# Optimization experiments

Measured on AMD Instinct MI355X. Metric: run time of the kernel, lower is better.

The kernel has to match this reference:

```python
import jax, jax.numpy as jnp
import numpy as np

NEG = jnp.float32(-1e9)


def setup_inputs() -> dict:
    key = jax.random.key(0)
    ks = jax.random.split(key, 8)
    B, S, D = 8, 2048, 1024
    scale = 1.0 / np.sqrt(D)
    return {
        "xQ": jax.random.normal(ks[0], (B, S, D), jnp.float32),
        "xK": jax.random.normal(ks[1], (B, S, D), jnp.float32),
        "xV": jax.random.normal(ks[2], (B, S, D), jnp.float32),
        "padding_mask": jax.random.randint(ks[3], (B, S), 0, 2, jnp.int32),
        "casual_mask": jnp.ones((B, S), jnp.int32),
        "W_q": jax.random.normal(ks[4], (D, D), jnp.float32) * scale,
        "b_q": jnp.zeros((D,), jnp.float32),
        "W_k": jax.random.normal(ks[5], (D, D), jnp.float32) * scale,
        "b_k": jnp.zeros((D,), jnp.float32),
        "W_v": jax.random.normal(ks[6], (D, D), jnp.float32) * scale,
        "b_v": jnp.zeros((D,), jnp.float32),
    }


def reference(xQ, xK, xV, padding_mask, casual_mask, W_q, b_q, W_k, b_k, W_v, b_v):
    # Linear projections (torch nn.Linear: x @ W.T + b)
    Q = jnp.einsum('bsd,ed->bse', xQ, W_q) + b_q
    K = jnp.einsum('bsd,ed->bse', xK, W_k) + b_k
    V = jnp.einsum('bsd,ed->bse', xV, W_v) + b_v

    # Raw logits (note: original code applies NO 1/sqrt(dk) scaling)
    QKT = jnp.einsum('bqd,bkd->bqk', Q, K)  # [B, Sq, Sk]

    # Additive padding mask: -1e9 on padded key positions
    pad = jnp.where(padding_mask[:, None, :] == 0, NEG, jnp.float32(0.0))
    # Additive causal mask: -1e9 above the diagonal
    Sq, Sk = QKT.shape[1], QKT.shape[2]
    caus = jnp.where(
        jnp.tril(jnp.ones((Sq, Sk), dtype=bool)), jnp.float32(0.0), NEG
    )[None, :, :]
    QKT = QKT + pad + caus

    S = jax.nn.softmax(QKT, axis=-1)
    return jnp.einsum('bqk,bkd->bqd', S, V)
```

## Files before the change

kernel.cpp:

```cpp
#include <hip/hip_runtime.h>

typedef __attribute__((ext_vector_type(4))) float f4;
typedef __attribute__((ext_vector_type(4))) float f32x4;
typedef _Float16 half4 __attribute__((ext_vector_type(4)));
typedef _Float16 half8 __attribute__((ext_vector_type(8)));

#define DEVI static __device__ __forceinline__

DEVI void gload_lds16(const void* g, void* l) {
  __builtin_amdgcn_global_load_lds(
      (const __attribute__((address_space(1))) void*)g,
      (__attribute__((address_space(3))) void*)l, 16, 0, 0);
}

#define STEP_SYNC()                                     \
  asm volatile("s_waitcnt vmcnt(0)" ::: "memory");      \
  __builtin_amdgcn_sched_barrier(0);                    \
  __builtin_amdgcn_s_barrier();                         \
  __builtin_amdgcn_sched_barrier(0);

DEVI int xcd_swz(int id, int n) {
  int q = n >> 3, r = n & 7;
  int x = id & 7, c = id >> 3;
  return (x < r ? x * (q + 1) : r * (q + 1) + (x - r) * q) + c;
}

template <int SL>
__global__ __launch_bounds__(256) void cvt_split(const float* __restrict__ X,
                                                 _Float16* __restrict__ H,
                                                 _Float16* __restrict__ L,
                                                 int n4) {
  int i = blockIdx.x * 256 + threadIdx.x;
  const int stride = gridDim.x * 256;
  for (; i < n4; i += stride) {
    f4 x = ((const f4*)X)[i];
    half4 h, l;
#pragma unroll
    for (int j = 0; j < 4; ++j) {
      h[j] = (_Float16)x[j];
      if (SL) l[j] = (_Float16)(x[j] - (float)h[j]);
    }
    ((half4*)H)[i] = h;
    if (SL) ((half4*)L)[i] = l;
  }
}

template <int AR, int BR, int ASPLIT, int BSPLIT>
DEVI void core(const _Float16* __restrict__ A0, const _Float16* __restrict__ A1,
               const _Float16* __restrict__ B0, const _Float16* __restrict__ B1,
               int lda, int ldb, int NS, _Float16* lds, f32x4 (&acc)[4][4]) {
  constexpr int WN = BR / 64;
  constexpr int ACH = AR * 32;
  constexpr int BCH = BR * 32;
  constexpr int CHUNK = ACH * (1 + ASPLIT) + BCH * (1 + BSPLIT);
  const int tid = threadIdx.x;
  const int w = tid >> 6, lane = tid & 63;
  const int wm = w / WN, wn = w % WN;
  const int r16 = lane & 15, kg = lane >> 4;

  auto STAGE = [&](int t) {
    _Float16* base = lds + (size_t)(t & 1) * CHUNK;
#pragma unroll
    for (int j = 0; j < AR / 128; ++j) {
      int g = j * 512 + tid;
      int row = g >> 2, c = g & 3;
      int cs = (c ^ (row >> 1)) & 3;
      size_t src = (size_t)row * lda + cs * 8 + t * 32;
      int dst = (j * 512 + w * 64) * 8;
      gload_lds16(A0 + src, base + dst);
      if (ASPLIT) gload_lds16(A1 + src, base + ACH + dst);
    }
    _Float16* bb = base + ACH * (1 + ASPLIT);
#pragma unroll
    for (int j = 0; j < BR / 128; ++j) {
      int g = j * 512 + tid;
      int row = g >> 2, c = g & 3;
      int cs = (c ^ (row >> 1)) & 3;
      size_t src = (size_t)row * ldb + cs * 8 + t * 32;
      int dst = (j * 512 + w * 64) * 8;
      gload_lds16(B0 + src, bb + dst);
      if (BSPLIT) gload_lds16(B1 + src, bb + BCH + dst);
    }
  };

  auto COMPUTE = [&](int t) {
    const _Float16* base = lds + (size_t)(t & 1) * CHUNK;
    const _Float16* la = base;
    const _Float16* lb = base + ACH * (1 + ASPLIT);
    half8 a0[4], a1[4], b0[4], b1[4];
#pragma unroll
    for (int mi = 0; mi < 4; ++mi) {
      int row = wm * 64 + mi * 16 + r16;
      int off = row * 32 + (((kg ^ (row >> 1)) & 3) * 8);
      a0[mi] = *(const half8*)(la + off);
      if (ASPLIT) a1[mi] = *(const half8*)(la + ACH + off);
    }
#pragma unroll
    for (int ni = 0; ni < 4; ++ni) {
      int row = wn * 64 + ni * 16 + r16;
      int off = row * 32 + (((kg ^ (row >> 1)) & 3) * 8);
      b0[ni] = *(const half8*)(lb + off);
      if (BSPLIT) b1[ni] = *(const half8*)(lb + BCH + off);
    }
    __builtin_amdgcn_s_setprio(1);
#pragma unroll
    for (int mi = 0; mi < 4; ++mi)
#pragma unroll
      for (int ni = 0; ni < 4; ++ni) {
        acc[mi][ni] = __builtin_amdgcn_mfma_f32_16x16x32_f16(
            a0[mi], b0[ni], acc[mi][ni], 0, 0, 0);
        if (ASPLIT)
          acc[mi][ni] = __builtin_amdgcn_mfma_f32_16x16x32_f16(
              a1[mi], b0[ni], acc[mi][ni], 0, 0, 0);
        if (BSPLIT)
          acc[mi][ni] = __builtin_amdgcn_mfma_f32_16x16x32_f16(
              a0[mi], b1[ni], acc[mi][ni], 0, 0, 0);
      }
    __builtin_amdgcn_s_setprio(0);
  };

  STAGE(0);
  STEP_SYNC();
  for (int t = 0; t < NS; ++t) {
    if (t + 1 < NS) STAGE(t + 1);
    COMPUTE(t);
    STEP_SYNC();
  }
}

DEVI void acc_zero(f32x4 (&acc)[4][4]) {
#pragma unroll
  for (int i = 0; i < 4; ++i)
#pragma unroll
    for (int j = 0; j < 4; ++j) acc[i][j] = (f32x4)0.0f;
}

template <int STORE_LO>
__global__ __launch_bounds__(512, 4) void proj_eng(
    const _Float16* __restrict__ X, const _Float16* __restrict__ Wh,
    const _Float16* __restrict__ Wl, const float* __restrict__ bias,
    _Float16* __restrict__ OutHi, _Float16* __restrict__ OutLo) {
  extern __shared__ _Float16 lds[];
  const int id = xcd_swz(blockIdx.x, gridDim.x);
  const int m0 = (id >> 3) * 256, n0 = (id & 7) * 128;
  f32x4 acc[4][4];
  acc_zero(acc);
  core<256, 128, 0, 1>(X + (size_t)m0 * 1024, nullptr,
                       Wh + (size_t)n0 * 1024, Wl + (size_t)n0 * 1024, 1024,
                       1024, 32, lds, acc);
  const int tid = threadIdx.x;
  const int w = tid >> 6, lane = tid & 63;
  const int wm = w >> 1, wn = w & 1;
  const int r16 = lane & 15, kg = lane >> 4;
  float bcol[4];
#pragma unroll
  for (int ni = 0; ni < 4; ++ni) bcol[ni] = bias[n0 + wn * 64 + ni * 16 + r16];
#pragma unroll
  for (int mi = 0; mi < 4; ++mi) {
    int row = m0 + wm * 64 + mi * 16 + kg * 4;
#pragma unroll
    for (int ni = 0; ni < 4; ++ni) {
      int col = n0 + wn * 64 + ni * 16 + r16;
#pragma unroll
      for (int j = 0; j < 4; ++j) {
        float v = acc[mi][ni][j] + bcol[ni];
        _Float16 h = (_Float16)v;
        OutHi[(size_t)(row + j) * 1024 + col] = h;
        if (STORE_LO)
          OutLo[(size_t)(row + j) * 1024 + col] = (_Float16)(v - (float)h);
      }
    }
  }
}

__global__ __launch_bounds__(512, 4) void proj_eng_v(
    const _Float16* __restrict__ X, const _Float16* __restrict__ Wh,
    const float* __restrict__ bias, _Float16* __restrict__ Vt) {
  extern __shared__ _Float16 lds[];
  const int id = xcd_swz(blockIdx.x, gridDim.x);
  const int m0 = (id >> 3) * 256, n0 = (id & 7) * 128;
  f32x4 acc[4][4];
  acc_zero(acc);
  core<256, 128, 0, 0>(X + (size_t)m0 * 1024, nullptr,
                       Wh + (size_t)n0 * 1024, nullptr, 1024, 1024, 32, lds,
                       acc);
  const int tid = threadIdx.x;
  const int w = tid >> 6, lane = tid & 63;
  const int wm = w >> 1, wn = w & 1;
  const int r16 = lane & 15, kg = lane >> 4;
  float bcol[4];
#pragma unroll
  for (int ni = 0; ni < 4; ++ni) bcol[ni] = bias[n0 + wn * 64 + ni * 16 + r16];
  __syncthreads();
  _Float16(*T)[256] = (_Float16(*)[256])lds;
#pragma unroll
  for (int mi = 0; mi < 4; ++mi) {
    int ml = wm * 64 + mi * 16 + kg * 4;
#pragma unroll
    for (int ni = 0; ni < 4; ++ni) {
      int nl = wn * 64 + ni * 16 + r16;
#pragma unroll
      for (int j = 0; j < 4; ++j)
        T[nl][ml + j] = (_Float16)(acc[mi][ni][j] + bcol[ni]);
    }
  }
  __syncthreads();
  const int b = m0 >> 11;
  const int s0 = m0 & 2047;
#pragma unroll
  for (int r = 0; r < 8; ++r) {
    int flat = tid + r * 512;
    int n = flat >> 5, c = flat & 31;
    half8 v = *(const half8*)&T[n][c * 8];
    *(half8*)(Vt + (size_t)b * (1024 * 2048) + (size_t)(n0 + n) * 2048 + s0 +
              c * 8) = v;
  }
}

__global__ __launch_bounds__(512, 4) void qk_eng(
    const _Float16* __restrict__ Qh, const _Float16* __restrict__ Ql,
    const _Float16* __restrict__ Kh, float* __restrict__ Lg, int bbase) {
  extern __shared__ _Float16 lds[];
  const int id = xcd_swz(blockIdx.x, gridDim.x);
  const int y = id / 72;
  int t = id % 72;
  int qt = 0, base = 0;
  while (t >= base + (qt >> 1) + 1) { base += (qt >> 1) + 1; ++qt; }
  const int kt = t - base;
  const int b = bbase + y;
  const size_t boff = (size_t)b * (2048 * 1024);
  f32x4 acc[4][4];
  acc_zero(acc);
  core<128, 256, 1, 0>(Qh + boff + (size_t)(qt * 128) * 1024,
                       Ql + boff + (size_t)(qt * 128) * 1024,
                       Kh + boff + (size_t)(kt * 256) * 1024, nullptr, 1024,
                       1024, 32, lds, acc);
  const int tid = threadIdx.x;
  const int w = tid >> 6, lane = tid & 63;
  const int wm = w >> 2, wn = w & 3;
  const int r16 = lane & 15, kg = lane >> 4;
  float* L = Lg + (size_t)y * (2048 * 2048);
#pragma unroll
  for (int mi = 0; mi < 4; ++mi) {
    int row = qt * 128 + wm * 64 + mi * 16 + kg * 4;
#pragma unroll
    for (int ni = 0; ni < 4; ++ni) {
      int col = kt * 256 + wn * 64 + ni * 16 + r16;
#pragma unroll
      for (int j = 0; j < 4; ++j)
        L[(size_t)(row + j) * 2048 + col] = acc[mi][ni][j];
    }
  }
}

__global__ __launch_bounds__(512, 4) void pv_eng(
    const float* __restrict__ Lg, const _Float16* __restrict__ Vt,
    float* __restrict__ Out, int bbase) {
  extern __shared__ _Float16 lds[];
  const int id = xcd_swz(blockIdx.x, gridDim.x);
  const int y = id >> 6;
  const int qt = (id & 63) >> 2, nt = id & 3;
  const int b = bbase + y;
  const _Float16* P = (const _Float16*)(Lg + (size_t)y * (2048 * 2048));
  f32x4 acc[4][4];
  acc_zero(acc);
  core<128, 256, 0, 0>(P + (size_t)(qt * 128) * 4096, nullptr,
                       Vt + (size_t)b * (1024 * 2048) + (size_t)(nt * 256) * 2048,
                       nullptr, 4096, 2048, ((qt >> 1) + 1) * 8, lds, acc);
  const int tid = threadIdx.x;
  const int w = tid >> 6, lane = tid & 63;
  const int wm = w >> 2, wn = w & 3;
  const int r16 = lane & 15, kg = lane >> 4;
#pragma unroll
  for (int mi = 0; mi < 4; ++mi) {
    int row = qt * 128 + wm * 64 + mi * 16 + kg * 4;
#pragma unroll
    for (int ni = 0; ni < 4; ++ni) {
      int col = nt * 256 + wn * 64 + ni * 16 + r16;
#pragma unroll
      for (int j = 0; j < 4; ++j)
        Out[(size_t)(b * 2048 + row + j) * 1024 + col] = acc[mi][ni][j];
    }
  }
}

template <int NSPLIT, int STORE_LO>
__global__ __launch_bounds__(256) void proj_kernel(
    const float* __restrict__ X, const float* __restrict__ W,
    const float* __restrict__ bias, _Float16* __restrict__ OutHi,
    _Float16* __restrict__ OutLo) {
  __shared__ struct {
    float As[128][36];
    float Bs[128][36];
  } u;
  const int tid = threadIdx.x;
  const int lane = tid & 63, w = tid >> 6;
  const int wm = w >> 1, wn = w & 1;
  const int r16 = lane & 15, kg = lane >> 4;
  const int m0 = blockIdx.y * 128, n0 = blockIdx.x * 128;
  f32x4 acc[4][4];
#pragma unroll
  for (int i = 0; i < 4; ++i)
#pragma unroll
    for (int j = 0; j < 4; ++j) acc[i][j] = (f32x4)0.0f;
  f4 ra[4], rb[4];
  auto LOAD = [&](int kt) {
#pragma unroll
    for (int r = 0; r < 4; ++r) {
      int flat = tid + r * 256;
      int row = flat >> 3, c = flat & 7;
      ra[r] = *(const f4*)(X + (size_t)(m0 + row) * 1024 + kt * 32 + c * 4);
      rb[r] = *(const f4*)(W + (size_t)(n0 + row) * 1024 + kt * 32 + c * 4);
    }
  };
  LOAD(0);
  for (int kt = 0; kt < 32; ++kt) {
    __syncthreads();
#pragma unroll
    for (int r = 0; r < 4; ++r) {
      int flat = tid + r * 256;
      int row = flat >> 3, c = flat & 7;
      *(f4*)&u.As[row][c * 4] = ra[r];
      *(f4*)&u.Bs[row][c * 4] = rb[r];
    }
    __syncthreads();
    if (kt + 1 < 32) LOAD(kt + 1);
    half8 ah[4], al[4], bh[4];
#pragma unroll
    for (int mi = 0; mi < 4; ++mi) {
      const float* p = &u.As[wm * 64 + mi * 16 + r16][kg * 8];
      f4 x0 = *(const f4*)p, x1 = *(const f4*)(p + 4);
      half8 h, l;
#pragma unroll
      for (int j = 0; j < 4; ++j) {
        h[j] = (_Float16)x0[j];
        h[j + 4] = (_Float16)x1[j];
      }
      ah[mi] = h;
      if (NSPLIT == 2) {
#pragma unroll
        for (int j = 0; j < 4; ++j) {
          l[j] = (_Float16)(x0[j] - (float)h[j]);
          l[j + 4] = (_Float16)(x1[j] - (float)h[j + 4]);
        }
        al[mi] = l;
      }
    }
#pragma unroll
    for (int ni = 0; ni < 4; ++ni) {
      const float* p = &u.Bs[wn * 64 + ni * 16 + r16][kg * 8];
      f4 x0 = *(const f4*)p, x1 = *(const f4*)(p + 4);
      half8 h;
#pragma unroll
      for (int j = 0; j < 4; ++j) {
        h[j] = (_Float16)x0[j];
        h[j + 4] = (_Float16)x1[j];
      }
      bh[ni] = h;
    }
#pragma unroll
    for (int mi = 0; mi < 4; ++mi)
#pragma unroll
      for (int ni = 0; ni < 4; ++ni) {
        acc[mi][ni] = __builtin_amdgcn_mfma_f32_16x16x32_f16(
            ah[mi], bh[ni], acc[mi][ni], 0, 0, 0);
        if (NSPLIT == 2)
          acc[mi][ni] = __builtin_amdgcn_mfma_f32_16x16x32_f16(
              al[mi], bh[ni], acc[mi][ni], 0, 0, 0);
      }
  }
  float bcol[4];
#pragma unroll
  for (int ni = 0; ni < 4; ++ni) bcol[ni] = bias[n0 + wn * 64 + ni * 16 + r16];
#pragma unroll
  for (int mi = 0; mi < 4; ++mi) {
    int row = m0 + wm * 64 + mi * 16 + kg * 4;
#pragma unroll
    for (int ni = 0; ni < 4; ++ni) {
      int col = n0 + wn * 64 + ni * 16 + r16;
#pragma unroll
      for (int j = 0; j < 4; ++j) {
        float v = acc[mi][ni][j] + bcol[ni];
        _Float16 h = (_Float16)v;
        OutHi[(size_t)(row + j) * 1024 + col] = h;
        if (STORE_LO)
          OutLo[(size_t)(row + j) * 1024 + col] = (_Float16)(v - (float)h);
      }
    }
  }
}

__global__ __launch_bounds__(256) void softmax_kernel(
    float* __restrict__ Lg, const int* __restrict__ pad, int bbase) {
  const int q = blockIdx.x;
  const int y = blockIdx.y;
  const int b = bbase + y;
  const int tid = threadIdx.x;
  float* row = Lg + (size_t)y * (2048 * 2048) + (size_t)q * 2048;
  _Float16* prow = (_Float16*)row;
  const int* pb = pad + (size_t)b * 2048;
  const int kend = ((q >> 8) + 1) << 8;
  float v[8];
  int nv = 0;
  float mx = -3.0e38f;
  for (int k = tid; k <= q; k += 256) {
    float l = row[k];
    if (pb[k] == 0) l += -1.0e9f;
    v[nv++] = l;
    mx = fmaxf(mx, l);
  }
  __shared__ float red[4];
  for (int o = 32; o; o >>= 1) mx = fmaxf(mx, __shfl_xor(mx, o));
  if ((tid & 63) == 0) red[tid >> 6] = mx;
  __syncthreads();
  mx = fmaxf(fmaxf(red[0], red[1]), fmaxf(red[2], red[3]));
  __syncthreads();
  float s = 0.f;
  for (int i = 0; i < nv; ++i) s += expf(v[i] - mx);
  for (int o = 32; o; o >>= 1) s += __shfl_xor(s, o);
  if ((tid & 63) == 0) red[tid >> 6] = s;
  __syncthreads();
  s = red[0] + red[1] + red[2] + red[3];
  const float inv = 1.0f / s;
  int i = 0;
  for (int k = tid; k <= q; k += 256) {
    prow[k] = (_Float16)(expf(v[i] - mx) * inv);
    ++i;
  }
  for (int k = q + 1 + tid; k < kend; k += 256) prow[k] = (_Float16)0.0f;
}

__global__ __launch_bounds__(512) void fix_f(const int* __restrict__ pad,
                                             int* __restrict__ fb) {
  const int b = threadIdx.x >> 6, k = threadIdx.x & 63;
  unsigned long long m = __ballot(pad[b * 2048 + k] != 0);
  if (k == 0) fb[b] = m ? (__ffsll((long long)m) - 1) : 64;
}

__global__ __launch_bounds__(256) void fix_qrow2(
    const float* __restrict__ xQ, const float* __restrict__ Wq,
    const float* __restrict__ bq, const int* __restrict__ fb,
    float* __restrict__ Qrow) {
  const int b = blockIdx.y;
  const int f = fb[b];
  const int tid = threadIdx.x;
  const int e = blockIdx.x * 16 + (tid >> 4);
  const int l16 = tid & 15;
  __shared__ float xq[1024];
  for (int q = 0; q < f; ++q) {
    *(f4*)&xq[tid * 4] = ((const f4*)(xQ + (size_t)(b * 2048 + q) * 1024))[tid];
    __syncthreads();
    float a = 0.f;
#pragma unroll
    for (int it = 0; it < 16; ++it) {
      int d = l16 * 4 + it * 64;
      f4 ww = *(const f4*)(Wq + (size_t)e * 1024 + d);
      a += xq[d] * ww[0] + xq[d + 1] * ww[1] + xq[d + 2] * ww[2] +
           xq[d + 3] * ww[3];
    }
    for (int o = 8; o; o >>= 1) a += __shfl_xor(a, o);
    if (l16 == 0) Qrow[((size_t)b * 64 + q) * 1024 + e] = a + bq[e];
    __syncthreads();
  }
}

__global__ __launch_bounds__(256) void fix_qb0(const float* __restrict__ bk,
                                               const int* __restrict__ fb,
                                               const float* __restrict__ Qrow,
                                               float* __restrict__ qb0) {
  const int q = blockIdx.x, b = blockIdx.y;
  if (q >= fb[b]) return;
  const int tid = threadIdx.x;
  const float* qr = Qrow + ((size_t)b * 64 + q) * 1024;
  float p = 0.f;
  for (int e = tid; e < 1024; e += 256) p += qr[e] * bk[e];
  __shared__ float red[4];
  for (int o = 32; o; o >>= 1) p += __shfl_xor(p, o);
  if ((tid & 63) == 0) red[tid >> 6] = p;
  __syncthreads();
  if (tid == 0) qb0[b * 64 + q] = red[0] + red[1] + red[2] + red[3];
}

__global__ __launch_bounds__(256) void fix_g2(const float* __restrict__ Wk,
                                              const int* __restrict__ fb,
                                              const float* __restrict__ Qrow,
                                              float* __restrict__ Gpart) {
  const int b = blockIdx.y;
  const int f = fb[b];
  const int tid = threadIdx.x;
  const int ddblk = blockIdx.x & 3, es = blockIdx.x >> 2;
  const int dd = ddblk * 256 + tid;
  __shared__ float qc[128];
  for (int q = 0; q < f; ++q) {
    if (tid < 32)
      *(f4*)&qc[tid * 4] =
          ((const f4*)(Qrow + ((size_t)b * 64 + q) * 1024 + es * 128))[tid];
    __syncthreads();
    float g = 0.f;
    for (int e = 0; e < 128; ++e)
      g += qc[e] * Wk[(size_t)(es * 128 + e) * 1024 + dd];
    Gpart[(((size_t)es * 8 + b) * 64 + q) * 1024 + dd] = g;
    __syncthreads();
  }
}

__global__ __launch_bounds__(256) void fix_logit2(
    const float* __restrict__ xK, const int* __restrict__ pad,
    const int* __restrict__ fb, const float* __restrict__ Gpart,
    const float* __restrict__ qb0, float* __restrict__ lrow) {
  const int b = blockIdx.y;
  const int f = fb[b];
  const int tid = threadIdx.x;
  const int k = blockIdx.x * 16 + (tid >> 4);
  const int l16 = tid & 15;
  __shared__ float Gs[1024];
  for (int q = 0; q < f; ++q) {
    f4 s = (f4)0.0f;
#pragma unroll
    for (int es = 0; es < 8; ++es)
      s += ((const f4*)(Gpart + (((size_t)es * 8 + b) * 64 + q) * 1024))[tid];
    *(f4*)&Gs[tid * 4] = s;
    __syncthreads();
    float a = 0.f;
#pragma unroll
    for (int it = 0; it < 16; ++it) {
      int d = l16 * 4 + it * 64;
      f4 x = *(const f4*)(xK + (size_t)(b * 2048 + k) * 1024 + d);
      a += x[0] * Gs[d] + x[1] * Gs[d + 1] + x[2] * Gs[d + 2] +
           x[3] * Gs[d + 3];
    }
    for (int o = 8; o; o >>= 1) a += __shfl_xor(a, o);
    if (l16 == 0) {
      float l = a + qb0[b * 64 + q];
      if (pad[b * 2048 + k] == 0) l += -1.0e9f;
      if (k > q) l += -1.0e9f;
      lrow[((size_t)b * 64 + q) * 2048 + k] = l;
    }
    __syncthreads();
  }
}

__global__ __launch_bounds__(256) void fix_sm(const int* __restrict__ fb,
                                              float* __restrict__ lrow,
                                              float* __restrict__ srow) {
  const int q = blockIdx.x, b = blockIdx.y;
  if (q >= fb[b]) return;
  const int tid = threadIdx.x;
  float* row = lrow + ((size_t)b * 64 + q) * 2048;
  float v[8];
  float mx = -3.0e38f;
#pragma unroll
  for (int i = 0; i < 8; ++i) {
    v[i] = row[tid + i * 256];
    mx = fmaxf(mx, v[i]);
  }
  __shared__ float red[4];
  for (int o = 32; o; o >>= 1) mx = fmaxf(mx, __shfl_xor(mx, o));
  if ((tid & 63) == 0) red[tid >> 6] = mx;
  __syncthreads();
  mx = fmaxf(fmaxf(red[0], red[1]), fmaxf(red[2], red[3]));
  __syncthreads();
  float s = 0.f;
#pragma unroll
  for (int i = 0; i < 8; ++i) {
    v[i] = expf(v[i] - mx);
    s += v[i];
  }
#pragma unroll
  for (int i = 0; i < 8; ++i) row[tid + i * 256] = v[i];
  for (int o = 32; o; o >>= 1) s += __shfl_xor(s, o);
  if ((tid & 63) == 0) red[tid >> 6] = s;
  __syncthreads();
  if (tid == 0) srow[b * 64 + q] = red[0] + red[1] + red[2] + red[3];
}

__global__ __launch_bounds__(256) void fix_pv2(
    const _Float16* __restrict__ Vt, const int* __restrict__ fb,
    const float* __restrict__ lrow, const float* __restrict__ srow,
    float* __restrict__ Out) {
  const int b = blockIdx.y;
  const int f = fb[b];
  const int tid = threadIdx.x;
  const int d = blockIdx.x * 16 + (tid >> 4);
  const int l16 = tid & 15;
  __shared__ float ps[2048];
  for (int q = 0; q < f; ++q) {
    const f4* src = (const f4*)(lrow + ((size_t)b * 64 + q) * 2048);
    *(f4*)&ps[tid * 8] = src[tid * 2];
    *(f4*)&ps[tid * 8 + 4] = src[tid * 2 + 1];
    __syncthreads();
    float o = 0.f;
#pragma unroll
    for (int it = 0; it < 16; ++it) {
      int k = l16 * 8 + it * 128;
      half8 vv = *(const half8*)(Vt + (size_t)b * (1024 * 2048) +
                                 (size_t)d * 2048 + k);
      o += (float)vv[0] * ps[k] + (float)vv[1] * ps[k + 1] +
           (float)vv[2] * ps[k + 2] + (float)vv[3] * ps[k + 3] +
           (float)vv[4] * ps[k + 4] + (float)vv[5] * ps[k + 5] +
           (float)vv[6] * ps[k + 6] + (float)vv[7] * ps[k + 7];
    }
    for (int of = 8; of; of >>= 1) o += __shfl_xor(o, of);
    if (l16 == 0)
      Out[(size_t)(b * 2048 + q) * 1024 + d] = o * (1.0f / srow[b * 64 + q]);
    __syncthreads();
  }
}

extern "C" void kernel_launch(void* const* d_in, const int* in_sizes, int n_in,
                              void* d_out, int out_size, void* d_ws,
                              size_t ws_size, hipStream_t stream) {
  const float* xQ = (const float*)d_in[0];
  const float* xK = (const float*)d_in[1];
  const float* xV = (const float*)d_in[2];
  const int* pad = (const int*)d_in[3];
  const float* Wq = (const float*)d_in[5];
  const float* bq = (const float*)d_in[6];
  const float* Wk = (const float*)d_in[7];
  const float* bk = (const float*)d_in[8];
  const float* Wv = (const float*)d_in[9];
  const float* bv = (const float*)d_in[10];
  float* Out = (float*)d_out;

  const size_t MB = (size_t)1 << 20;
  char* wsb = (char*)d_ws;
  _Float16* Qh = (_Float16*)(wsb);
  _Float16* Ql = (_Float16*)(wsb + 32 * MB);
  _Float16* Kh = (_Float16*)(wsb + 64 * MB);
  _Float16* Vt = (_Float16*)(wsb + 96 * MB);
  float* Lg = (float*)(wsb + 128 * MB);

  size_t avail = (ws_size > 128 * MB) ? ws_size - 128 * MB : 0;
  int G = (int)(avail / (16 * MB));
  if (G > 8) G = 8;
  if (G < 1) G = 1;

  const int SM_PROJ = 65536, SM_V = 65536, SM_QK = 65536, SM_PV = 49152;
  (void)hipFuncSetAttribute((const void*)&proj_eng<1>,
                            hipFuncAttributeMaxDynamicSharedMemorySize, SM_PROJ);
  (void)hipFuncSetAttribute((const void*)&proj_eng<0>,
                            hipFuncAttributeMaxDynamicSharedMemorySize, SM_PROJ);
  (void)hipFuncSetAttribute((const void*)&proj_eng_v,
                            hipFuncAttributeMaxDynamicSharedMemorySize, SM_V);
  (void)hipFuncSetAttribute((const void*)&qk_eng,
                            hipFuncAttributeMaxDynamicSharedMemorySize, SM_QK);
  (void)hipFuncSetAttribute((const void*)&pv_eng,
                            hipFuncAttributeMaxDynamicSharedMemorySize, SM_PV);

  dim3 blk(256), eblk(512);

  {
    _Float16* sX = (_Float16*)(wsb);
    _Float16* sW = (_Float16*)(wsb + 32 * MB);
    cvt_split<0><<<dim3(2048), blk, 0, stream>>>(xV, sX, nullptr, 4194304);
    cvt_split<0><<<dim3(1024), blk, 0, stream>>>(Wv, sW, nullptr, 262144);
    proj_eng_v<<<dim3(512), eblk, SM_V, stream>>>(sX, sW, bv, Vt);
  }
  {
    _Float16* sX = (_Float16*)(wsb);
    _Float16* sWh = (_Float16*)(wsb + 32 * MB);
    _Float16* sWl = (_Float16*)(wsb + 34 * MB);
    cvt_split<0><<<dim3(2048), blk, 0, stream>>>(xK, sX, nullptr, 4194304);
    cvt_split<1><<<dim3(1024), blk, 0, stream>>>(Wk, sWh, sWl, 262144);
    proj_eng<0><<<dim3(512), eblk, SM_PROJ, stream>>>(sX, sWh, sWl, bk, Kh,
                                                      nullptr);
  }
  if (ws_size >= 166 * MB) {
    _Float16* sX = (_Float16*)(wsb + 128 * MB);
    _Float16* sWh = (_Float16*)(wsb + 160 * MB);
    _Float16* sWl = (_Float16*)(wsb + 162 * MB);
    cvt_split<0><<<dim3(2048), blk, 0, stream>>>(xQ, sX, nullptr, 4194304);
    cvt_split<1><<<dim3(1024), blk, 0, stream>>>(Wq, sWh, sWl, 262144);
    proj_eng<1><<<dim3(512), eblk, SM_PROJ, stream>>>(sX, sWh, sWl, bq, Qh, Ql);
  } else {
    proj_kernel<2, 1><<<dim3(8, 128), blk, 0, stream>>>(xQ, Wq, bq, Qh, Ql);
  }

  for (int bbase = 0; bbase < 8; bbase += G) {
    int nb = (8 - bbase < G) ? (8 - bbase) : G;
    qk_eng<<<dim3(72 * nb), eblk, SM_QK, stream>>>(Qh, Ql, Kh, Lg, bbase);
    softmax_kernel<<<dim3(2048, nb), blk, 0, stream>>>(Lg, pad, bbase);
    pv_eng<<<dim3(64 * nb), eblk, SM_PV, stream>>>(Lg, Vt, Out, bbase);
  }

  int* fb = (int*)(wsb);
  float* qb0 = (float*)(wsb + 4 * 1024);
  float* srow = (float*)(wsb + 8 * 1024);
  float* Qrow = (float*)(wsb + 1 * MB);
  float* Gpart = (float*)(wsb + 4 * MB);
  float* lrow = (float*)(wsb + 20 * MB);

  fix_f<<<dim3(1), dim3(512), 0, stream>>>(pad, fb);
  fix_qrow2<<<dim3(64, 8), blk, 0, stream>>>(xQ, Wq, bq, fb, Qrow);
  fix_qb0<<<dim3(64, 8), blk, 0, stream>>>(bk, fb, Qrow, qb0);
  fix_g2<<<dim3(32, 8), blk, 0, stream>>>(Wk, fb, Qrow, Gpart);
  fix_logit2<<<dim3(128, 8), blk, 0, stream>>>(xK, pad, fb, Gpart, qb0, lrow);
  fix_sm<<<dim3(64, 8), blk, 0, stream>>>(fb, lrow, srow);
  fix_pv2<<<dim3(64, 8), blk, 0, stream>>>(Vt, fb, lrow, srow, Out);
}
```

Before: 497.7 us.

## Interleave hi/lo fp16 splits along K and triple-buffer the GEMM core

Split-fp16 operands are now stored interleaved, with hi and lo adjacent along K, and weights duplicated to match. A single MFMA stream over a doubled K then replaces the separate hi/lo loads and extra MFMAs. The shared GEMM core moves from double to triple buffering with a partial vmcnt wait, so loads can stay in flight across iterations. This doubles K-loop length and buffer footprint (72KB LDS, larger workspace) and may reduce occupancy. It keeps roughly the same MFMA count while removing separate split-buffer loads.

```diff
diff --git a/kernel.cpp b/kernel.cpp
--- a/kernel.cpp
+++ b/kernel.cpp
@@ -2,7 +2,6 @@
 
 typedef __attribute__((ext_vector_type(4))) float f4;
 typedef __attribute__((ext_vector_type(4))) float f32x4;
-typedef _Float16 half4 __attribute__((ext_vector_type(4)));
 typedef _Float16 half8 __attribute__((ext_vector_type(8)));
 
 #define DEVI static __device__ __forceinline__
@@ -13,11 +12,11 @@
       (__attribute__((address_space(3))) void*)l, 16, 0, 0);
 }
 
-#define STEP_SYNC()                                     \
-  asm volatile("s_waitcnt vmcnt(0)" ::: "memory");      \
-  __builtin_amdgcn_sched_barrier(0);                    \
-  __builtin_amdgcn_s_barrier();                         \
-  __builtin_amdgcn_sched_barrier(0);
+DEVI unsigned int pack2(_Float16 a, _Float16 b) {
+  unsigned short ua = __builtin_bit_cast(unsigned short, a);
+  unsigned short ub = __builtin_bit_cast(unsigned short, b);
+  return (unsigned int)ua | ((unsigned int)ub << 16);
+}
 
 DEVI int xcd_swz(int id, int n) {
   int q = n >> 3, r = n & 7;
@@ -25,107 +24,113 @@
   return (x < r ? x * (q + 1) : r * (q + 1) + (x - r) * q) + c;
 }
 
-template <int SL>
-__global__ __launch_bounds__(256) void cvt_split(const float* __restrict__ X,
+#define FENCED_BARRIER()                \
+  __builtin_amdgcn_sched_barrier(0);    \
+  __builtin_amdgcn_s_barrier();         \
+  __builtin_amdgcn_sched_barrier(0);
+
+__global__ __launch_bounds__(256) void cvt_plain(const float* __restrict__ X,
                                                  _Float16* __restrict__ H,
-                                                 _Float16* __restrict__ L,
                                                  int n4) {
+  int i = blockIdx.x * 256 + threadIdx.x;
+  const int stride = gridDim.x * 256;
+  typedef _Float16 half4v __attribute__((ext_vector_type(4)));
+  for (; i < n4; i += stride) {
+    f4 x = ((const f4*)X)[i];
+    half4v h;
+#pragma unroll
+    for (int j = 0; j < 4; ++j) h[j] = (_Float16)x[j];
+    ((half4v*)H)[i] = h;
+  }
+}
+
+template <int DUP>
+__global__ __launch_bounds__(256) void cvt_wide(const float* __restrict__ X,
+                                                _Float16* __restrict__ H,
+                                                int n4) {
   int i = blockIdx.x * 256 + threadIdx.x;
   const int stride = gridDim.x * 256;
   for (; i < n4; i += stride) {
     f4 x = ((const f4*)X)[i];
-    half4 h, l;
+    half8 o;
 #pragma unroll
     for (int j = 0; j < 4; ++j) {
-      h[j] = (_Float16)x[j];
-      if (SL) l[j] = (_Float16)(x[j] - (float)h[j]);
-    }
-    ((half4*)H)[i] = h;
-    if (SL) ((half4*)L)[i] = l;
-  }
-}
-
-template <int AR, int BR, int ASPLIT, int BSPLIT>
-DEVI void core(const _Float16* __restrict__ A0, const _Float16* __restrict__ A1,
-               const _Float16* __restrict__ B0, const _Float16* __restrict__ B1,
+      _Float16 h = (_Float16)x[j];
+      o[2 * j] = h;
+      o[2 * j + 1] = DUP ? h : (_Float16)(x[j] - (float)h);
+    }
+    ((half8*)H)[i] = o;
+  }
+}
+
+template <int AR, int BR>
+DEVI void core(const _Float16* __restrict__ A0, const _Float16* __restrict__ B0,
                int lda, int ldb, int NS, _Float16* lds, f32x4 (&acc)[4][4]) {
   constexpr int WN = BR / 64;
   constexpr int ACH = AR * 32;
-  constexpr int BCH = BR * 32;
-  constexpr int CHUNK = ACH * (1 + ASPLIT) + BCH * (1 + BSPLIT);
+  constexpr int CHUNK = (AR + BR) * 32;
   const int tid = threadIdx.x;
   const int w = tid >> 6, lane = tid & 63;
   const int wm = w / WN, wn = w % WN;
   const int r16 = lane & 15, kg = lane >> 4;
 
-  auto STAGE = [&](int t) {
-    _Float16* base = lds + (size_t)(t & 1) * CHUNK;
+  auto STAGE = [&](int t, int buf) {
+    _Float16* base = lds + buf * CHUNK;
 #pragma unroll
     for (int j = 0; j < AR / 128; ++j) {
       int g = j * 512 + tid;
       int row = g >> 2, c = g & 3;
       int cs = (c ^ (row >> 1)) & 3;
-      size_t src = (size_t)row * lda + cs * 8 + t * 32;
-      int dst = (j * 512 + w * 64) * 8;
-      gload_lds16(A0 + src, base + dst);
-      if (ASPLIT) gload_lds16(A1 + src, base + ACH + dst);
-    }
-    _Float16* bb = base + ACH * (1 + ASPLIT);
+      gload_lds16(A0 + (size_t)row * lda + t * 32 + cs * 8,
+                  base + (j * 512 + w * 64) * 8);
+    }
+    _Float16* bb = base + ACH;
 #pragma unroll
     for (int j = 0; j < BR / 128; ++j) {
       int g = j * 512 + tid;
       int row = g >> 2, c = g & 3;
       int cs = (c ^ (row >> 1)) & 3;
-      size_t src = (size_t)row * ldb + cs * 8 + t * 32;
-      int dst = (j * 512 + w * 64) * 8;
-      gload_lds16(B0 + src, bb + dst);
-      if (BSPLIT) gload_lds16(B1 + src, bb + BCH + dst);
+      gload_lds16(B0 + (size_t)row * ldb + t * 32 + cs * 8,
+                  bb + (j * 512 + w * 64) * 8);
     }
   };
 
-  auto COMPUTE = [&](int t) {
-    const _Float16* base = lds + (size_t)(t & 1) * CHUNK;
-    const _Float16* la = base;
-    const _Float16* lb = base + ACH * (1 + ASPLIT);
-    half8 a0[4], a1[4], b0[4], b1[4];
+  auto COMPUTE = [&](int buf) {
+    const _Float16* la = lds + buf * CHUNK;
+    const _Float16* lb = la + ACH;
+    half8 a[4], b[4];
 #pragma unroll
     for (int mi = 0; mi < 4; ++mi) {
       int row = wm * 64 + mi * 16 + r16;
-      int off = row * 32 + (((kg ^ (row >> 1)) & 3) * 8);
-      a0[mi] = *(const half8*)(la + off);
-      if (ASPLIT) a1[mi] = *(const half8*)(la + ACH + off);
+      a[mi] = *(const half8*)(la + row * 32 + (((kg ^ (row >> 1)) & 3) * 8));
     }
 #pragma unroll
     for (int ni = 0; ni < 4; ++ni) {
       int row = wn * 64 + ni * 16 + r16;
-      int off = row * 32 + (((kg ^ (row >> 1)) & 3) * 8);
-      b0[ni] = *(const half8*)(lb + off);
-      if (BSPLIT) b1[ni] = *(const half8*)(lb + BCH + off);
+      b[ni] = *(const half8*)(lb + row * 32 + (((kg ^ (row >> 1)) & 3) * 8));
     }
     __builtin_amdgcn_s_setprio(1);
 #pragma unroll
     for (int mi = 0; mi < 4; ++mi)
 #pragma unroll
-      for (int ni = 0; ni < 4; ++ni) {
+      for (int ni = 0; ni < 4; ++ni)
         acc[mi][ni] = __builtin_amdgcn_mfma_f32_16x16x32_f16(
-            a0[mi], b0[ni], acc[mi][ni], 0, 0, 0);
-        if (ASPLIT)
-          acc[mi][ni] = __builtin_amdgcn_mfma_f32_16x16x32_f16(
-              a1[mi], b0[ni], acc[mi][ni], 0, 0, 0);
-        if (BSPLIT)
-          acc[mi][ni] = __builtin_amdgcn_mfma_f32_16x16x32_f16(
-              a0[mi], b1[ni], acc[mi][ni], 0, 0, 0);
-      }
+            a[mi], b[ni], acc[mi][ni], 0, 0, 0);
     __builtin_amdgcn_s_setprio(0);
   };
 
-  STAGE(0);
-  STEP_SYNC();
-  for (int t = 0; t < NS; ++t) {
-    if (t + 1 < NS) STAGE(t + 1);
-    COMPUTE(t);
-    STEP_SYNC();
-  }
+  STAGE(0, 0);
+  STAGE(1, 1);
+  int t = 0;
+  for (; t < NS - 1; ++t) {
+    asm volatile("s_waitcnt vmcnt(3)" ::: "memory");
+    FENCED_BARRIER();
+    if (t + 2 < NS) STAGE(t + 2, (t + 2) % 3);
+    COMPUTE(t % 3);
+  }
+  asm volatile("s_waitcnt vmcnt(0)" ::: "memory");
+  FENCED_BARRIER();
+  COMPUTE(t % 3);
 }
 
 DEVI void acc_zero(f32x4 (&acc)[4][4]) {
@@ -135,19 +140,17 @@
     for (int j = 0; j < 4; ++j) acc[i][j] = (f32x4)0.0f;
 }
 
-template <int STORE_LO>
+template <int OUTMODE>
 __global__ __launch_bounds__(512, 4) void proj_eng(
-    const _Float16* __restrict__ X, const _Float16* __restrict__ Wh,
-    const _Float16* __restrict__ Wl, const float* __restrict__ bias,
-    _Float16* __restrict__ OutHi, _Float16* __restrict__ OutLo) {
+    const _Float16* __restrict__ Xi, const _Float16* __restrict__ Wd,
+    const float* __restrict__ bias, unsigned int* __restrict__ OutU) {
   extern __shared__ _Float16 lds[];
   const int id = xcd_swz(blockIdx.x, gridDim.x);
   const int m0 = (id >> 3) * 256, n0 = (id & 7) * 128;
   f32x4 acc[4][4];
   acc_zero(acc);
-  core<256, 128, 0, 1>(X + (size_t)m0 * 1024, nullptr,
-                       Wh + (size_t)n0 * 1024, Wl + (size_t)n0 * 1024, 1024,
-                       1024, 32, lds, acc);
+  core<256, 128>(Xi + (size_t)m0 * 2048, Wd + (size_t)n0 * 2048, 2048, 2048,
+                 64, lds, acc);
   const int tid = threadIdx.x;
   const int w = tid >> 6, lane = tid & 63;
   const int wm = w >> 1, wn = w & 1;
@@ -165,9 +168,8 @@
       for (int j = 0; j < 4; ++j) {
         float v = acc[mi][ni][j] + bcol[ni];
         _Float16 h = (_Float16)v;
-        OutHi[(size_t)(row + j) * 1024 + col] = h;
-        if (STORE_LO)
-          OutLo[(size_t)(row + j) * 1024 + col] = (_Float16)(v - (float)h);
+        _Float16 x2 = OUTMODE ? h : (_Float16)(v - (float)h);
+        OutU[(size_t)(row + j) * 1024 + col] = pack2(h, x2);
       }
     }
   }
@@ -181,9 +183,8 @@
   const int m0 = (id >> 3) * 256, n0 = (id & 7) * 128;
   f32x4 acc[4][4];
   acc_zero(acc);
-  core<256, 128, 0, 0>(X + (size_t)m0 * 1024, nullptr,
-                       Wh + (size_t)n0 * 1024, nullptr, 1024, 1024, 32, lds,
-                       acc);
+  core<256, 128>(X + (size_t)m0 * 1024, Wh + (size_t)n0 * 1024, 1024, 1024, 32,
+                 lds, acc);
   const int tid = threadIdx.x;
   const int w = tid >> 6, lane = tid & 63;
   const int wm = w >> 1, wn = w & 1;
@@ -218,8 +219,8 @@
 }
 
 __global__ __launch_bounds__(512, 4) void qk_eng(
-    const _Float16* __restrict__ Qh, const _Float16* __restrict__ Ql,
-    const _Float16* __restrict__ Kh, float* __restrict__ Lg, int bbase) {
+    const _Float16* __restrict__ Qi, const _Float16* __restrict__ Kd,
+    float* __restrict__ Lg, int bbase) {
   extern __shared__ _Float16 lds[];
   const int id = xcd_swz(blockIdx.x, gridDim.x);
   const int y = id / 72;
@@ -228,13 +229,11 @@
   while (t >= base + (qt >> 1) + 1) { base += (qt >> 1) + 1; ++qt; }
   const int kt = t - base;
   const int b = bbase + y;
-  const size_t boff = (size_t)b * (2048 * 1024);
   f32x4 acc[4][4];
   acc_zero(acc);
-  core<128, 256, 1, 0>(Qh + boff + (size_t)(qt * 128) * 1024,
-                       Ql + boff + (size_t)(qt * 128) * 1024,
-                       Kh + boff + (size_t)(kt * 256) * 1024, nullptr, 1024,
-                       1024, 32, lds, acc);
+  core<128, 256>(Qi + ((size_t)b * 2048 + qt * 128) * 2048,
+                 Kd + ((size_t)b * 2048 + kt * 256) * 2048, 2048, 2048, 64,
+                 lds, acc);
   const int tid = threadIdx.x;
   const int w = tid >> 6, lane = tid & 63;
   const int wm = w >> 2, wn = w & 3;
@@ -264,9 +263,9 @@
   const _Float16* P = (const _Float16*)(Lg + (size_t)y * (2048 * 2048));
   f32x4 acc[4][4];
   acc_zero(acc);
-  core<128, 256, 0, 0>(P + (size_t)(qt * 128) * 4096, nullptr,
-                       Vt + (size_t)b * (1024 * 2048) + (size_t)(nt * 256) * 2048,
-                       nullptr, 4096, 2048, ((qt >> 1) + 1) * 8, lds, acc);
+  core<128, 256>(P + (size_t)(qt * 128) * 4096,
+                 Vt + (size_t)b * (1024 * 2048) + (size_t)(nt * 256) * 2048,
+                 4096, 2048, ((qt >> 1) + 1) * 8, lds, acc);
   const int tid = threadIdx.x;
   const int w = tid >> 6, lane = tid & 63;
   const int wm = w >> 2, wn = w & 3;
@@ -284,11 +283,10 @@
   }
 }
 
-template <int NSPLIT, int STORE_LO>
-__global__ __launch_bounds__(256) void proj_kernel(
+template <int OUTMODE>
+__global__ __launch_bounds__(256) void proj_legacy(
     const float* __restrict__ X, const float* __restrict__ W,
-    const float* __restrict__ bias, _Float16* __restrict__ OutHi,
-    _Float16* __restrict__ OutLo) {
+    const float* __restrict__ bias, unsigned int* __restrict__ OutU) {
   __shared__ struct {
     float As[128][36];
     float Bs[128][36];
@@ -299,10 +297,7 @@
   const int r16 = lane & 15, kg = lane >> 4;
   const int m0 = blockIdx.y * 128, n0 = blockIdx.x * 128;
   f32x4 acc[4][4];
-#pragma unroll
-  for (int i = 0; i < 4; ++i)
-#pragma unroll
-    for (int j = 0; j < 4; ++j) acc[i][j] = (f32x4)0.0f;
+  acc_zero(acc);
   f4 ra[4], rb[4];
   auto LOAD = [&](int kt) {
 #pragma unroll
@@ -335,16 +330,11 @@
       for (int j = 0; j < 4; ++j) {
         h[j] = (_Float16)x0[j];
         h[j + 4] = (_Float16)x1[j];
+        l[j] = (_Float16)(x0[j] - (float)h[j]);
+        l[j + 4] = (_Float16)(x1[j] - (float)h[j + 4]);
       }
       ah[mi] = h;
-      if (NSPLIT == 2) {
-#pragma unroll
-        for (int j = 0; j < 4; ++j) {
-          l[j] = (_Float16)(x0[j] - (float)h[j]);
-          l[j + 4] = (_Float16)(x1[j] - (float)h[j + 4]);
-        }
-        al[mi] = l;
-      }
+      al[mi] = l;
     }
 #pragma unroll
     for (int ni = 0; ni < 4; ++ni) {
@@ -364,9 +354,8 @@
       for (int ni = 0; ni < 4; ++ni) {
         acc[mi][ni] = __builtin_amdgcn_mfma_f32_16x16x32_f16(
             ah[mi], bh[ni], acc[mi][ni], 0, 0, 0);
-        if (NSPLIT == 2)
-          acc[mi][ni] = __builtin_amdgcn_mfma_f32_16x16x32_f16(
-              al[mi], bh[ni], acc[mi][ni], 0, 0, 0);
+        acc[mi][ni] = __builtin_amdgcn_mfma_f32_16x16x32_f16(
+            al[mi], bh[ni], acc[mi][ni], 0, 0, 0);
       }
   }
   float bcol[4];
@@ -382,9 +371,8 @@
       for (int j = 0; j < 4; ++j) {
         float v = acc[mi][ni][j] + bcol[ni];
         _Float16 h = (_Float16)v;
-        OutHi[(size_t)(row + j) * 1024 + col] = h;
-        if (STORE_LO)
-          OutLo[(size_t)(row + j) * 1024 + col] = (_Float16)(v - (float)h);
+        _Float16 x2 = OUTMODE ? h : (_Float16)(v - (float)h);
+        OutU[(size_t)(row + j) * 1024 + col] = pack2(h, x2);
       }
     }
   }
@@ -624,63 +612,63 @@
 
   const size_t MB = (size_t)1 << 20;
   char* wsb = (char*)d_ws;
-  _Float16* Qh = (_Float16*)(wsb);
-  _Float16* Ql = (_Float16*)(wsb + 32 * MB);
-  _Float16* Kh = (_Float16*)(wsb + 64 * MB);
-  _Float16* Vt = (_Float16*)(wsb + 96 * MB);
-  float* Lg = (float*)(wsb + 128 * MB);
-
-  size_t avail = (ws_size > 128 * MB) ? ws_size - 128 * MB : 0;
+  _Float16* Qi = (_Float16*)(wsb);
+  _Float16* Kd = (_Float16*)(wsb + 64 * MB);
+  _Float16* Vt = (_Float16*)(wsb + 128 * MB);
+  float* Lg = (float*)(wsb + 160 * MB);
+
+  size_t avail = (ws_size > 160 * MB) ? ws_size - 160 * MB : 0;
   int G = (int)(avail / (16 * MB));
   if (G > 8) G = 8;
   if (G < 1) G = 1;
 
-  const int SM_PROJ = 65536, SM_V = 65536, SM_QK = 65536, SM_PV = 49152;
+  const int SMEM = 73728;
+  (void)hipFuncSetAttribute((const void*)&proj_eng<0>,
+                            hipFuncAttributeMaxDynamicSharedMemorySize, SMEM);
   (void)hipFuncSetAttribute((const void*)&proj_eng<1>,
-                            hipFuncAttributeMaxDynamicSharedMemorySize, SM_PROJ);
-  (void)hipFuncSetAttribute((const void*)&proj_eng<0>,
-                            hipFuncAttributeMaxDynamicSharedMemorySize, SM_PROJ);
+                            hipFuncAttributeMaxDynamicSharedMemorySize, SMEM);
   (void)hipFuncSetAttribute((const void*)&proj_eng_v,
-                            hipFuncAttributeMaxDynamicSharedMemorySize, SM_V);
+                            hipFuncAttributeMaxDynamicSharedMemorySize, SMEM);
   (void)hipFuncSetAttribute((const void*)&qk_eng,
-                            hipFuncAttributeMaxDynamicSharedMemorySize, SM_QK);
+                            hipFuncAttributeMaxDynamicSharedMemorySize, SMEM);
   (void)hipFuncSetAttribute((const void*)&pv_eng,
-                            hipFuncAttributeMaxDynamicSharedMemorySize, SM_PV);
+                            hipFuncAttributeMaxDynamicSharedMemorySize, SMEM);
 
   dim3 blk(256), eblk(512);
+  const bool fast = (ws_size >= 228 * MB);
 
   {
     _Float16* sX = (_Float16*)(wsb);
     _Float16* sW = (_Float16*)(wsb + 32 * MB);
-    cvt_split<0><<<dim3(2048), blk, 0, stream>>>(xV, sX, nullptr, 4194304);
-    cvt_split<0><<<dim3(1024), blk, 0, stream>>>(Wv, sW, nullptr, 262144);
-    proj_eng_v<<<dim3(512), eblk, SM_V, stream>>>(sX, sW, bv, Vt);
-  }
-  {
-    _Float16* sX = (_Float16*)(wsb);
-    _Float16* sWh = (_Float16*)(wsb + 32 * MB);
-    _Float16* sWl = (_Float16*)(wsb + 34 * MB);
-    cvt_split<0><<<dim3(2048), blk, 0, stream>>>(xK, sX, nullptr, 4194304);
-    cvt_split<1><<<dim3(1024), blk, 0, stream>>>(Wk, sWh, sWl, 262144);
-    proj_eng<0><<<dim3(512), eblk, SM_PROJ, stream>>>(sX, sWh, sWl, bk, Kh,
-                                                      nullptr);
-  }
-  if (ws_size >= 166 * MB) {
-    _Float16* sX = (_Float16*)(wsb + 128 * MB);
-    _Float16* sWh = (_Float16*)(wsb + 160 * MB);
-    _Float16* sWl = (_Float16*)(wsb + 162 * MB);
-    cvt_split<0><<<dim3(2048), blk, 0, stream>>>(xQ, sX, nullptr, 4194304);
-    cvt_split<1><<<dim3(1024), blk, 0, stream>>>(Wq, sWh, sWl, 262144);
-    proj_eng<1><<<dim3(512), eblk, SM_PROJ, stream>>>(sX, sWh, sWl, bq, Qh, Ql);
+    cvt_plain<<<dim3(2048), blk, 0, stream>>>(xV, sX, 4194304);
+    cvt_plain<<<dim3(1024), blk, 0, stream>>>(Wv, sW, 262144);
+    proj_eng_v<<<dim3(512), eblk, SMEM, stream>>>(sX, sW, bv, Vt);
+  }
+  if (fast) {
+    _Float16* XiK = (_Float16*)(wsb);
+    _Float16* WdK = (_Float16*)(wsb + 160 * MB);
+    cvt_wide<0><<<dim3(2048), blk, 0, stream>>>(xK, XiK, 4194304);
+    cvt_wide<1><<<dim3(1024), blk, 0, stream>>>(Wk, WdK, 262144);
+    proj_eng<1><<<dim3(512), eblk, SMEM, stream>>>(XiK, WdK, bk,
+                                                   (unsigned int*)Kd);
+    _Float16* XiQ = (_Float16*)(wsb + 160 * MB);
+    _Float16* WdQ = (_Float16*)(wsb + 224 * MB);
+    cvt_wide<0><<<dim3(2048), blk, 0, stream>>>(xQ, XiQ, 4194304);
+    cvt_wide<1><<<dim3(1024), blk, 0, stream>>>(Wq, WdQ, 262144);
+    proj_eng<0><<<dim3(512), eblk, SMEM, stream>>>(XiQ, WdQ, bq,
+                                                   (unsigned int*)Qi);
   } else {
-    proj_kernel<2, 1><<<dim3(8, 128), blk, 0, stream>>>(xQ, Wq, bq, Qh, Ql);
+    proj_legacy<1><<<dim3(8, 128), blk, 0, stream>>>(xK, Wk, bk,
+                                                     (unsigned int*)Kd);
+    proj_legacy<0><<<dim3(8, 128), blk, 0, stream>>>(xQ, Wq, bq,
+                                                     (unsigned int*)Qi);
   }
 
   for (int bbase = 0; bbase < 8; bbase += G) {
     int nb = (8 - bbase < G) ? (8 - bbase) : G;
-    qk_eng<<<dim3(72 * nb), eblk, SM_QK, stream>>>(Qh, Ql, Kh, Lg, bbase);
+    qk_eng<<<dim3(72 * nb), eblk, SMEM, stream>>>(Qi, Kd, Lg, bbase);
     softmax_kernel<<<dim3(2048, nb), blk, 0, stream>>>(Lg, pad, bbase);
-    pv_eng<<<dim3(64 * nb), eblk, SM_PV, stream>>>(Lg, Vt, Out, bbase);
+    pv_eng<<<dim3(64 * nb), eblk, SMEM, stream>>>(Lg, Vt, Out, bbase);
   }
 
   int* fb = (int*)(wsb);
```

Measured after the change: 603.3 us. 21.2% more time.
